# Kernel optimization log

Measured on AMD Instinct MI355X. Metric: run time of the kernel, lower is better.

Reference implementation:

```python
import jax, jax.numpy as jnp
import numpy as np

N = 4_194_304      # total points = num_clusters * avg points per cluster
C = 65_536         # number of clusters
FEATS = [64, 128, 256]


def setup_inputs() -> dict:
    key = jax.random.key(0)
    ks = jax.random.split(key, 8)
    points = jax.random.normal(ks[0], (N, 3), dtype=jnp.float32)
    cluster = jnp.sort(jax.random.randint(ks[1], (N,), 0, C, dtype=jnp.int64))
    dims = [3] + FEATS
    params = {}
    for i in range(3):
        fan_in = dims[i]
        scale = 1.0 / np.sqrt(fan_in)
        params[f"W{i}"] = (jax.random.uniform(ks[2 + 2 * i], (dims[i], dims[i + 1]),
                                              dtype=jnp.float32, minval=-1.0, maxval=1.0) * scale)
        params[f"b{i}"] = (jax.random.uniform(ks[3 + 2 * i], (dims[i + 1],),
                                              dtype=jnp.float32, minval=-1.0, maxval=1.0) * scale)
    return dict(points=points, cluster=cluster, **params)


def reference(points, cluster, W0, b0, W1, b1, W2, b2):
    # per-point fc0 + relu: [N,3] -> [N,64]
    h = jax.nn.relu(points @ W0 + b0)
    # cluster-wise max pool (pool_index == 1): [N,64] -> [C,64]
    pooled = jax.ops.segment_max(h, cluster, num_segments=C, indices_are_sorted=True)
    # empty clusters give -inf; PyG's scatter-max fills empty segments with 0
    pooled = jnp.where(jnp.isfinite(pooled), pooled, 0.0)
    # cluster-wise fc1, fc2 with relu
    h = jax.nn.relu(pooled @ W1 + b1)   # [C,128]
    h = jax.nn.relu(h @ W2 + b2)        # [C,256]
    return h
```

## Files before the change

### kernel.cpp

```cpp
#include <hip/hip_runtime.h>

#define N_PTS  (4*1024*1024)
#define NCLUST 65536

__global__ __launch_bounds__(256) void k_zero(float4* __restrict__ p)
{
    p[(size_t)blockIdx.x * 256 + threadIdx.x] = make_float4(0.f, 0.f, 0.f, 0.f);
}

__global__ __launch_bounds__(256) void k_fc0_pool(
        const float* __restrict__ pts,
        const int* __restrict__ clus,
        const float* __restrict__ W0,
        const float* __restrict__ b0,
        float* __restrict__ pooled)
{
    const int tid  = threadIdx.x;
    const int lane = tid & 63;
    const int w    = tid >> 6;
    const int base = blockIdx.x * 1024 + w * 256;

    const float w0x = W0[lane];
    const float w0y = W0[64 + lane];
    const float w0z = W0[128 + lane];
    const float bb  = b0[lane];

    unsigned* pool_u = (unsigned*)pooled;
    int   cur  = clus[base];
    float vmax = 0.0f;

#define FLUSH(RID) { \
    atomicMax(&pool_u[(size_t)(RID) * 64 + lane], __float_as_uint(vmax)); \
    vmax = 0.0f; }

#define RL_F(v, i) __uint_as_float(__builtin_amdgcn_readlane(__float_as_uint(v), (i)))

    #pragma unroll 1
    for (int rnd = 0; rnd < 4; ++rnd) {
        const int rb = base + rnd * 64;
        const float* ps = pts + (size_t)rb * 3;
        const float vx = ps[lane * 3 + 0];
        const float vy = ps[lane * 3 + 1];
        const float vz = ps[lane * 3 + 2];
        const int   vc = clus[rb + lane];

        #pragma unroll
        for (int ch = 0; ch < 4; ++ch) {
            const int i0 = ch * 16;
            const int cf = __builtin_amdgcn_readlane(vc, i0);
            const int cl = __builtin_amdgcn_readlane(vc, i0 + 15);
            if (cf == cl) {
                if (cf != cur) { FLUSH(cur); cur = cf; }
                float m0 = vmax, m1 = vmax, m2 = vmax, m3 = vmax;
                #pragma unroll
                for (int t = 0; t < 16; t += 4) {
                    const float ax = RL_F(vx, i0 + t),     ay = RL_F(vy, i0 + t),     az = RL_F(vz, i0 + t);
                    const float bx = RL_F(vx, i0 + t + 1), by = RL_F(vy, i0 + t + 1), bz = RL_F(vz, i0 + t + 1);
                    const float cx = RL_F(vx, i0 + t + 2), cy = RL_F(vy, i0 + t + 2), cz = RL_F(vz, i0 + t + 2);
                    const float dx = RL_F(vx, i0 + t + 3), dy = RL_F(vy, i0 + t + 3), dz = RL_F(vz, i0 + t + 3);
                    m0 = fmaxf(m0, fmaf(ax, w0x, fmaf(ay, w0y, fmaf(az, w0z, bb))));
                    m1 = fmaxf(m1, fmaf(bx, w0x, fmaf(by, w0y, fmaf(bz, w0z, bb))));
                    m2 = fmaxf(m2, fmaf(cx, w0x, fmaf(cy, w0y, fmaf(cz, w0z, bb))));
                    m3 = fmaxf(m3, fmaf(dx, w0x, fmaf(dy, w0y, fmaf(dz, w0z, bb))));
                }
                vmax = fmaxf(fmaxf(m0, m1), fmaxf(m2, m3));
            } else {
                #pragma unroll 1
                for (int t = 0; t < 16; ++t) {
                    const int c = __builtin_amdgcn_readlane(vc, i0 + t);
                    if (c != cur) { FLUSH(cur); cur = c; }
                    const float sx = RL_F(vx, i0 + t);
                    const float sy = RL_F(vy, i0 + t);
                    const float sz = RL_F(vz, i0 + t);
                    vmax = fmaxf(vmax, fmaf(sx, w0x, fmaf(sy, w0y, fmaf(sz, w0z, bb))));
                }
            }
        }
    }
    FLUSH(cur);
#undef FLUSH
#undef RL_F
}

__global__ __launch_bounds__(512, 4) void k_mlp(
        const float* __restrict__ pooled,
        const float* __restrict__ W1,
        const float* __restrict__ b1,
        const float* __restrict__ W2,
        const float* __restrict__ b2,
        float* __restrict__ out)
{
    __shared__ float Ps[64 * 65];
    __shared__ float Hs[64 * 129];

    const int tid  = threadIdx.x;
    const int lane = tid & 63;
    const int w    = __builtin_amdgcn_readfirstlane(tid >> 6);
    const int r0b  = blockIdx.x * 64;

    {
        const float4* src = (const float4*)(pooled + (size_t)r0b * 64);
        #pragma unroll
        for (int j = 0; j < 2; ++j) {
            const int m  = tid + 512 * j;
            const float4 v = src[m];
            const int r = m >> 4, c4 = m & 15;
            float* d = &Ps[r * 65 + c4 * 4];
            d[0] = v.x; d[1] = v.y; d[2] = v.z; d[3] = v.w;
        }
    }
    __syncthreads();

    {
        const int cb = w * 16;
        float accA[16];
        #pragma unroll
        for (int j = 0; j < 4; ++j) {
            const float4 b = *(const float4*)(b1 + cb + 4 * j);
            accA[4*j+0] = b.x; accA[4*j+1] = b.y; accA[4*j+2] = b.z; accA[4*j+3] = b.w;
        }
        #pragma unroll 2
        for (int k = 0; k < 64; ++k) {
            const float h = Ps[lane * 65 + k];
            const float4 wa = *(const float4*)(W1 + k * 128 + cb);
            const float4 wb = *(const float4*)(W1 + k * 128 + cb + 4);
            const float4 wc = *(const float4*)(W1 + k * 128 + cb + 8);
            const float4 wd = *(const float4*)(W1 + k * 128 + cb + 12);
            accA[ 0] = fmaf(h, wa.x, accA[ 0]);
            accA[ 1] = fmaf(h, wa.y, accA[ 1]);
            accA[ 2] = fmaf(h, wa.z, accA[ 2]);
            accA[ 3] = fmaf(h, wa.w, accA[ 3]);
            accA[ 4] = fmaf(h, wb.x, accA[ 4]);
            accA[ 5] = fmaf(h, wb.y, accA[ 5]);
            accA[ 6] = fmaf(h, wb.z, accA[ 6]);
            accA[ 7] = fmaf(h, wb.w, accA[ 7]);
            accA[ 8] = fmaf(h, wc.x, accA[ 8]);
            accA[ 9] = fmaf(h, wc.y, accA[ 9]);
            accA[10] = fmaf(h, wc.z, accA[10]);
            accA[11] = fmaf(h, wc.w, accA[11]);
            accA[12] = fmaf(h, wd.x, accA[12]);
            accA[13] = fmaf(h, wd.y, accA[13]);
            accA[14] = fmaf(h, wd.z, accA[14]);
            accA[15] = fmaf(h, wd.w, accA[15]);
        }
        #pragma unroll
        for (int j = 0; j < 16; ++j)
            Hs[lane * 129 + cb + j] = fmaxf(accA[j], 0.0f);
    }
    __syncthreads();

    float acc[32];
    const int cb2 = w * 32;
    #pragma unroll
    for (int j = 0; j < 8; ++j) {
        const float4 b = *(const float4*)(b2 + cb2 + 4 * j);
        acc[4*j+0] = b.x; acc[4*j+1] = b.y; acc[4*j+2] = b.z; acc[4*j+3] = b.w;
    }
    #pragma unroll 2
    for (int k = 0; k < 128; ++k) {
        const float h = Hs[lane * 129 + k];
        #pragma unroll
        for (int j = 0; j < 8; ++j) {
            const float4 wv = *(const float4*)(W2 + (size_t)k * 256 + cb2 + 4 * j);
            acc[4*j+0] = fmaf(h, wv.x, acc[4*j+0]);
            acc[4*j+1] = fmaf(h, wv.y, acc[4*j+1]);
            acc[4*j+2] = fmaf(h, wv.z, acc[4*j+2]);
            acc[4*j+3] = fmaf(h, wv.w, acc[4*j+3]);
        }
    }
    #pragma unroll
    for (int j = 0; j < 32; ++j) acc[j] = fmaxf(acc[j], 0.0f);

    #pragma unroll 1
    for (int s = 0; s < 2; ++s) {
        __syncthreads();
        if ((w >> 2) == s) {
            const int cl = cb2 - s * 128;
            #pragma unroll
            for (int j = 0; j < 32; ++j)
                Hs[lane * 129 + cl + j] = acc[j];
        }
        __syncthreads();
        #pragma unroll
        for (int it = 0; it < 4; ++it) {
            const int m = tid + 512 * it;
            const int r = m >> 5, c4 = m & 31;
            float4 o;
            o.x = Hs[r * 129 + c4 * 4 + 0];
            o.y = Hs[r * 129 + c4 * 4 + 1];
            o.z = Hs[r * 129 + c4 * 4 + 2];
            o.w = Hs[r * 129 + c4 * 4 + 3];
            *(float4*)(out + (size_t)(r0b + r) * 256 + s * 128 + c4 * 4) = o;
        }
    }
}

extern "C" void kernel_launch(void* const* d_in, const int* in_sizes, int n_in,
                              void* d_out, int out_size, void* d_ws, size_t ws_size,
                              hipStream_t stream) {
    const float* points  = (const float*)d_in[0];
    const int*   cluster = (const int*)d_in[1];
    const float* W0      = (const float*)d_in[2];
    const float* b0      = (const float*)d_in[3];
    const float* W1      = (const float*)d_in[4];
    const float* b1      = (const float*)d_in[5];
    const float* W2      = (const float*)d_in[6];
    const float* b2      = (const float*)d_in[7];
    float* out = (float*)d_out;

    float* pooled = (float*)d_ws;

    k_zero<<<(NCLUST * 64 / 4) / 256, 256, 0, stream>>>((float4*)pooled);
    k_fc0_pool<<<N_PTS / 1024, 256, 0, stream>>>(points, cluster, W0, b0, pooled);
    k_mlp<<<NCLUST / 64, 512, 0, stream>>>(pooled, W1, b1, W2, b2, out);
}
```

Baseline: 253.1 us.

## Retile MLP kernel to 16-row blocks with register tiles over rows and columns

```diff
diff --git a/kernel.cpp b/kernel.cpp
--- a/kernel.cpp
+++ b/kernel.cpp
@@ -82,7 +82,7 @@
 #undef RL_F
 }
 
-__global__ __launch_bounds__(512, 4) void k_mlp(
+__global__ __launch_bounds__(256, 8) void k_mlp(
         const float* __restrict__ pooled,
         const float* __restrict__ W1,
         const float* __restrict__ b1,
@@ -90,107 +90,95 @@
         const float* __restrict__ b2,
         float* __restrict__ out)
 {
-    __shared__ float Ps[64 * 65];
-    __shared__ float Hs[64 * 129];
-
-    const int tid  = threadIdx.x;
-    const int lane = tid & 63;
-    const int w    = __builtin_amdgcn_readfirstlane(tid >> 6);
-    const int r0b  = blockIdx.x * 64;
+    __shared__ float Ps[16 * 64];
+    __shared__ float Hs[16 * 132];
+
+    const int tid = threadIdx.x;
+    const int r0  = blockIdx.x * 16;
+
+    ((float4*)Ps)[tid] = ((const float4*)(pooled + (size_t)r0 * 64))[tid];
+    __syncthreads();
 
     {
-        const float4* src = (const float4*)(pooled + (size_t)r0b * 64);
-        #pragma unroll
-        for (int j = 0; j < 2; ++j) {
-            const int m  = tid + 512 * j;
-            const float4 v = src[m];
-            const int r = m >> 4, c4 = m & 15;
-            float* d = &Ps[r * 65 + c4 * 4];
-            d[0] = v.x; d[1] = v.y; d[2] = v.z; d[3] = v.w;
+        const int cq = tid & 31;
+        const int rg = tid >> 5;
+        const float4 bv = ((const float4*)b1)[cq];
+        float acc[2][4];
+        #pragma unroll
+        for (int r = 0; r < 2; ++r) {
+            acc[r][0] = bv.x; acc[r][1] = bv.y; acc[r][2] = bv.z; acc[r][3] = bv.w;
+        }
+        const float4* W1g = (const float4*)W1;
+        const float4* Ps4 = (const float4*)Ps;
+        #pragma unroll 4
+        for (int k4 = 0; k4 < 16; ++k4) {
+            float4 wv[4], pv[2];
+            #pragma unroll
+            for (int kk = 0; kk < 4; ++kk) wv[kk] = W1g[(k4 * 4 + kk) * 32 + cq];
+            #pragma unroll
+            for (int rr = 0; rr < 2; ++rr) pv[rr] = Ps4[(rg * 2 + rr) * 16 + k4];
+            #pragma unroll
+            for (int rr = 0; rr < 2; ++rr) {
+                const float* p = (const float*)&pv[rr];
+                #pragma unroll
+                for (int kk = 0; kk < 4; ++kk) {
+                    const float* wq = (const float*)&wv[kk];
+                    acc[rr][0] = fmaf(p[kk], wq[0], acc[rr][0]);
+                    acc[rr][1] = fmaf(p[kk], wq[1], acc[rr][1]);
+                    acc[rr][2] = fmaf(p[kk], wq[2], acc[rr][2]);
+                    acc[rr][3] = fmaf(p[kk], wq[3], acc[rr][3]);
+                }
+            }
+        }
+        #pragma unroll
+        for (int rr = 0; rr < 2; ++rr) {
+            float* d = &Hs[(rg * 2 + rr) * 132 + cq * 4];
+            d[0] = fmaxf(acc[rr][0], 0.0f);
+            d[1] = fmaxf(acc[rr][1], 0.0f);
+            d[2] = fmaxf(acc[rr][2], 0.0f);
+            d[3] = fmaxf(acc[rr][3], 0.0f);
         }
     }
     __syncthreads();
 
     {
-        const int cb = w * 16;
-        float accA[16];
-        #pragma unroll
-        for (int j = 0; j < 4; ++j) {
-            const float4 b = *(const float4*)(b1 + cb + 4 * j);
-            accA[4*j+0] = b.x; accA[4*j+1] = b.y; accA[4*j+2] = b.z; accA[4*j+3] = b.w;
-        }
+        const int cg = tid & 63;
+        const int rg = tid >> 6;
+        const float4 bv = ((const float4*)b2)[cg];
+        float acc[4][4];
+        #pragma unroll
+        for (int r = 0; r < 4; ++r) {
+            acc[r][0] = bv.x; acc[r][1] = bv.y; acc[r][2] = bv.z; acc[r][3] = bv.w;
+        }
+        const float4* W2g = (const float4*)W2;
         #pragma unroll 2
-        for (int k = 0; k < 64; ++k) {
-            const float h = Ps[lane * 65 + k];
-            const float4 wa = *(const float4*)(W1 + k * 128 + cb);
-            const float4 wb = *(const float4*)(W1 + k * 128 + cb + 4);
-            const float4 wc = *(const float4*)(W1 + k * 128 + cb + 8);
-            const float4 wd = *(const float4*)(W1 + k * 128 + cb + 12);
-            accA[ 0] = fmaf(h, wa.x, accA[ 0]);
-            accA[ 1] = fmaf(h, wa.y, accA[ 1]);
-            accA[ 2] = fmaf(h, wa.z, accA[ 2]);
-            accA[ 3] = fmaf(h, wa.w, accA[ 3]);
-            accA[ 4] = fmaf(h, wb.x, accA[ 4]);
-            accA[ 5] = fmaf(h, wb.y, accA[ 5]);
-            accA[ 6] = fmaf(h, wb.z, accA[ 6]);
-            accA[ 7] = fmaf(h, wb.w, accA[ 7]);
-            accA[ 8] = fmaf(h, wc.x, accA[ 8]);
-            accA[ 9] = fmaf(h, wc.y, accA[ 9]);
-            accA[10] = fmaf(h, wc.z, accA[10]);
-            accA[11] = fmaf(h, wc.w, accA[11]);
-            accA[12] = fmaf(h, wd.x, accA[12]);
-            accA[13] = fmaf(h, wd.y, accA[13]);
-            accA[14] = fmaf(h, wd.z, accA[14]);
-            accA[15] = fmaf(h, wd.w, accA[15]);
-        }
-        #pragma unroll
-        for (int j = 0; j < 16; ++j)
-            Hs[lane * 129 + cb + j] = fmaxf(accA[j], 0.0f);
-    }
-    __syncthreads();
-
-    float acc[32];
-    const int cb2 = w * 32;
-    #pragma unroll
-    for (int j = 0; j < 8; ++j) {
-        const float4 b = *(const float4*)(b2 + cb2 + 4 * j);
-        acc[4*j+0] = b.x; acc[4*j+1] = b.y; acc[4*j+2] = b.z; acc[4*j+3] = b.w;
-    }
-    #pragma unroll 2
-    for (int k = 0; k < 128; ++k) {
-        const float h = Hs[lane * 129 + k];
-        #pragma unroll
-        for (int j = 0; j < 8; ++j) {
-            const float4 wv = *(const float4*)(W2 + (size_t)k * 256 + cb2 + 4 * j);
-            acc[4*j+0] = fmaf(h, wv.x, acc[4*j+0]);
-            acc[4*j+1] = fmaf(h, wv.y, acc[4*j+1]);
-            acc[4*j+2] = fmaf(h, wv.z, acc[4*j+2]);
-            acc[4*j+3] = fmaf(h, wv.w, acc[4*j+3]);
-        }
-    }
-    #pragma unroll
-    for (int j = 0; j < 32; ++j) acc[j] = fmaxf(acc[j], 0.0f);
-
-    #pragma unroll 1
-    for (int s = 0; s < 2; ++s) {
-        __syncthreads();
-        if ((w >> 2) == s) {
-            const int cl = cb2 - s * 128;
-            #pragma unroll
-            for (int j = 0; j < 32; ++j)
-                Hs[lane * 129 + cl + j] = acc[j];
-        }
-        __syncthreads();
-        #pragma unroll
-        for (int it = 0; it < 4; ++it) {
-            const int m = tid + 512 * it;
-            const int r = m >> 5, c4 = m & 31;
+        for (int k4 = 0; k4 < 32; ++k4) {
+            float4 hv[4];
+            #pragma unroll
+            for (int rr = 0; rr < 4; ++rr)
+                hv[rr] = *(const float4*)&Hs[(rg * 4 + rr) * 132 + k4 * 4];
+            #pragma unroll
+            for (int kk = 0; kk < 4; ++kk) {
+                const float4 wv = W2g[(k4 * 4 + kk) * 64 + cg];
+                #pragma unroll
+                for (int rr = 0; rr < 4; ++rr) {
+                    const float hk = ((const float*)&hv[rr])[kk];
+                    acc[rr][0] = fmaf(hk, wv.x, acc[rr][0]);
+                    acc[rr][1] = fmaf(hk, wv.y, acc[rr][1]);
+                    acc[rr][2] = fmaf(hk, wv.z, acc[rr][2]);
+                    acc[rr][3] = fmaf(hk, wv.w, acc[rr][3]);
+                }
+            }
+        }
+        float4* out4 = (float4*)out;
+        #pragma unroll
+        for (int rr = 0; rr < 4; ++rr) {
             float4 o;
-            o.x = Hs[r * 129 + c4 * 4 + 0];
-            o.y = Hs[r * 129 + c4 * 4 + 1];
-            o.z = Hs[r * 129 + c4 * 4 + 2];
-            o.w = Hs[r * 129 + c4 * 4 + 3];
-            *(float4*)(out + (size_t)(r0b + r) * 256 + s * 128 + c4 * 4) = o;
+            o.x = fmaxf(acc[rr][0], 0.0f);
+            o.y = fmaxf(acc[rr][1], 0.0f);
+            o.z = fmaxf(acc[rr][2], 0.0f);
+            o.w = fmaxf(acc[rr][3], 0.0f);
+            out4[(size_t)(r0 + rg * 4 + rr) * 64 + cg] = o;
         }
     }
 }
@@ -212,5 +200,5 @@
 
     k_zero<<<(NCLUST * 64 / 4) / 256, 256, 0, stream>>>((float4*)pooled);
     k_fc0_pool<<<N_PTS / 1024, 256, 0, stream>>>(points, cluster, W0, b0, pooled);
-    k_mlp<<<NCLUST / 64, 512, 0, stream>>>(pooled, W1, b1, W2, b2, out);
-}
+    k_mlp<<<NCLUST / 16, 256, 0, stream>>>(pooled, W1, b1, W2, b2, out);
+}
```

Result: slower. 276.4 us (+9.2%).
